# Kernel tuning notes

Hardware: AMD Instinct MI355X
Metric: run time of the kernel (lower is better)

Reference implementation:

```python
import jax, jax.numpy as jnp
import numpy as np
import math

L_MAX = 2; NRAD = 8; R_CUT = 3.5; N_LAYERS = 4; MUL0 = 32; MUL1 = 16
N_NODES = 20000; N_EDGES = 640000

# Orthonormal (Frobenius) basis of symmetric traceless 3x3 matrices for l=2
# component order: xy, yz, z^2, xz, x^2-y^2
_s2 = 1.0 / math.sqrt(2.0); _s6 = 1.0 / math.sqrt(6.0)
_B = np.zeros((5, 3, 3), dtype=np.float32)
_B[0, 0, 1] = _B[0, 1, 0] = _s2
_B[1, 1, 2] = _B[1, 2, 1] = _s2
_B[2, 0, 0] = _B[2, 1, 1] = -_s6; _B[2, 2, 2] = 2 * _s6
_B[3, 0, 2] = _B[3, 2, 0] = _s2
_B[4, 0, 0] = _s2; _B[4, 1, 1] = -_s2
B2 = jnp.asarray(_B)


def silu(x):
    return x * jax.nn.sigmoid(x)


def cutoff_fn(d):
    # CosineCutoff
    return 0.5 * (jnp.cos(d * math.pi / R_CUT) + 1.0) * (d < R_CUT).astype(d.dtype)


def smearing(d, means, betas):
    # ExpNormalSmearing with CosineCutoff envelope
    dc = jnp.clip(d, 1e-6, R_CUT)[:, None]          # [E,1]
    a = 5.0 / R_CUT
    b = jnp.clip(betas, 1e-6, None)
    return cutoff_fn(dc) * jnp.exp(-b * (jnp.exp(-a * dc) - means) ** 2)  # [E,NRAD]


def sph_harm(rh):
    # real spherical harmonics up to l=2, component normalization, (x,y,z) l=1 order
    y0 = jnp.ones_like(rh[:, :1])
    y1 = math.sqrt(3.0) * rh                                   # [E,3]
    rr = rh[:, :, None] * rh[:, None, :]                       # [E,3,3]
    tr = (rh * rh).sum(-1) / 3.0
    rr = rr - tr[:, None, None] * jnp.eye(3, dtype=rh.dtype)   # traceless
    y2 = math.sqrt(15.0) * jnp.einsum('eij,kij->ek', rr, B2)   # [E,5]
    return jnp.concatenate([y0, y1, y2], axis=-1)              # [E,9]


def _forward(pos, alpha, atom_emb, ne_emb, ne_dw, ne_db, ne_cw, ne_cb,
             means, betas, rad_w1, rad_b1, rad_w2, rad_b2,
             tp_w00, tp_w110, tp_w01, tp_w10, tp_w12,
             self_ws, self_wv, pre_ws, pre_wv, post_ws, post_wv,
             ln_g, ln_b, g_w1, g_b1, g_w2, g_b2, z, edge_index):
    N = pos.shape[0]
    src, dst = edge_index[0], edge_index[1]
    rvec = pos[dst] - pos[src]
    d = jnp.sqrt((rvec * rvec).sum(-1) + 1e-12)                # [E]
    rhat = rvec / d[:, None]

    rbf = smearing(d, means, betas)                            # [E,NRAD]
    # per-l radial coefficients (3 small MLPs, stacked on leading dim)
    h = silu(jnp.einsum('en,lnh->leh', rbf, rad_w1) + rad_b1[:, None, :])
    coeff = jnp.einsum('leh,lho->leo', h, rad_w2) + rad_b2[:, None, :]  # [3,E,1]

    Y = sph_harm(rhat)                                         # [E,9]
    eattr = jnp.concatenate([Y[:, :1] * coeff[0],
                             Y[:, 1:4] * coeff[1],
                             Y[:, 4:9] * coeff[2]], axis=-1)
    eattr = jnp.nan_to_num(eattr, nan=0.0, posinf=0.0, neginf=0.0)

    # AtomEncoder + NeighborEmbedding
    s = atom_emb[z]                                            # [N,32]
    C = cutoff_fn(d)
    W = (rbf @ ne_dw + ne_db) * C[:, None]                     # [E,32]
    xn = ne_emb[z]
    aggr = jax.ops.segment_sum(xn[dst] * W, src, num_segments=N)
    s = jnp.concatenate([s, aggr], axis=-1) @ ne_cw + ne_cb    # [N,32]
    v = jnp.zeros((N, MUL1, 3), dtype=s.dtype)                 # l=1 features

    e0, e1, e2 = eattr[:, :1], eattr[:, 1:4], eattr[:, 4:9]
    Qe = jnp.einsum('ek,kij->eij', e2, B2)                     # l=2 as sym traceless matrix

    for li in range(N_LAYERS):
        ss, vs = s[src], v[src]
        # CG tensor product paths (FullyConnectedTensorProduct node x edge -> node)
        m_s = (ss * e0) @ tp_w00[li] + jnp.einsum('evc,ec->ev', vs, e1) @ tp_w110[li]
        m_v = (jnp.einsum('ei,io->eo', ss, tp_w01[li])[:, :, None] * e1[:, None, :]
               + jnp.einsum('evc,vo->eoc', vs * e0[:, :, None], tp_w10[li])
               + jnp.einsum('evc,vo->eoc', jnp.einsum('eij,evj->evi', Qe, vs), tp_w12[li]))
        # alpha-weighted scatter-add aggregation
        ms = jax.ops.segment_sum(m_s * alpha, dst, num_segments=N)
        mv = jax.ops.segment_sum(m_v * alpha[:, :, None], dst, num_segments=N)
        # self interaction (o3.Linear, block-diag per l)
        s = s @ self_ws[li] + ms
        v = jnp.einsum('nvc,vo->noc', v, self_wv[li]) + mv
        # pre-linear -> gate -> post-linear
        ps = s @ pre_ws[li]                                    # [N,48] scalars+gates
        pv = jnp.einsum('nvc,vo->noc', v, pre_wv[li])
        sc = silu(ps[:, :MUL0])
        g = jax.nn.sigmoid(ps[:, MUL0:])
        v = pv * g[:, :, None]
        s = sc @ post_ws[li]
        v = jnp.einsum('nvc,vo->noc', v, post_wv[li])
        # layernorm on scalar channels
        mu = s.mean(-1, keepdims=True)
        var = ((s - mu) ** 2).mean(-1, keepdims=True)
        s = (s - mu) / jnp.sqrt(var + 1e-5) * ln_g[li] + ln_b[li]
        # geom2s: vector norms -> scalar residual
        vn = jnp.sqrt((v * v).sum(-1) + 1e-12)                 # [N,16]
        delta = silu(vn @ g_w1[li] + g_b1[li]) @ g_w2[li] + g_b2[li]
        s = s + delta
    return jnp.concatenate([s, v.reshape(N, MUL1 * 3)], axis=-1)  # [N,80]


def setup_inputs() -> dict:
    key = jax.random.key(0)
    ks = jax.random.split(key, 40)
    f32 = jnp.float32

    def rn(k, shape, fan):
        return jax.random.normal(k, shape, dtype=f32) / math.sqrt(fan)

    start = math.exp(-R_CUT)
    inp = {
        'pos': jax.random.uniform(ks[0], (N_NODES, 3), dtype=f32) * 10.0,
        'alpha': jax.random.uniform(ks[1], (N_EDGES, 1), dtype=f32),
        'atom_emb': rn(ks[2], (100, MUL0), 1.0),
        'ne_emb': rn(ks[3], (100, MUL0), 1.0),
        'ne_dw': rn(ks[4], (NRAD, MUL0), NRAD), 'ne_db': jnp.zeros((MUL0,), f32),
        'ne_cw': rn(ks[5], (2 * MUL0, MUL0), 2 * MUL0), 'ne_cb': jnp.zeros((MUL0,), f32),
        'means': jnp.linspace(start, 1.0, NRAD, dtype=f32),
        'betas': jnp.full((NRAD,), (2.0 / NRAD * (1.0 - start)) ** (-2), dtype=f32),
        'rad_w1': rn(ks[6], (3, NRAD, 256), NRAD), 'rad_b1': jnp.zeros((3, 256), f32),
        'rad_w2': rn(ks[7], (3, 256, 1), 256), 'rad_b2': jnp.zeros((3, 1), f32),
        'tp_w00': rn(ks[8], (N_LAYERS, MUL0, MUL0), MUL0),
        'tp_w110': rn(ks[9], (N_LAYERS, MUL1, MUL0), MUL1),
        'tp_w01': rn(ks[10], (N_LAYERS, MUL0, MUL1), MUL0),
        'tp_w10': rn(ks[11], (N_LAYERS, MUL1, MUL1), MUL1),
        'tp_w12': rn(ks[12], (N_LAYERS, MUL1, MUL1), MUL1),
        'self_ws': rn(ks[13], (N_LAYERS, MUL0, MUL0), MUL0),
        'self_wv': rn(ks[14], (N_LAYERS, MUL1, MUL1), MUL1),
        'pre_ws': rn(ks[15], (N_LAYERS, MUL0, MUL0 + MUL1), MUL0),
        'pre_wv': rn(ks[16], (N_LAYERS, MUL1, MUL1), MUL1),
        'post_ws': rn(ks[17], (N_LAYERS, MUL0, MUL0), MUL0),
        'post_wv': rn(ks[18], (N_LAYERS, MUL1, MUL1), MUL1),
        'ln_g': jnp.ones((N_LAYERS, MUL0), f32), 'ln_b': jnp.zeros((N_LAYERS, MUL0), f32),
        'g_w1': rn(ks[19], (N_LAYERS, MUL1, MUL1), MUL1), 'g_b1': jnp.zeros((N_LAYERS, MUL1), f32),
        'g_w2': rn(ks[20], (N_LAYERS, MUL1, MUL0), MUL1), 'g_b2': jnp.zeros((N_LAYERS, MUL0), f32),
        'z': jax.random.randint(ks[21], (N_NODES,), 0, 100, dtype=jnp.int32),
        'edge_index': jax.random.randint(ks[22], (2, N_EDGES), 0, N_NODES, dtype=jnp.int32),
    }
    return inp


def reference(pos, alpha, atom_emb, ne_emb, ne_dw, ne_db, ne_cw, ne_cb,
              means, betas, rad_w1, rad_b1, rad_w2, rad_b2,
              tp_w00, tp_w110, tp_w01, tp_w10, tp_w12,
              self_ws, self_wv, pre_ws, pre_wv, post_ws, post_wv,
              ln_g, ln_b, g_w1, g_b1, g_w2, g_b2, z, edge_index):
    return _forward(pos, alpha, atom_emb, ne_emb, ne_dw, ne_db, ne_cw, ne_cb,
                    means, betas, rad_w1, rad_b1, rad_w2, rad_b2,
                    tp_w00, tp_w110, tp_w01, tp_w10, tp_w12,
                    self_ws, self_wv, pre_ws, pre_wv, post_ws, post_wv,
                    ln_g, ln_b, g_w1, g_b1, g_w2, g_b2, z, edge_index)
```

## Files before the change

### kernel.cpp

```cpp
#include <hip/hip_runtime.h>

#define RCUT 3.5f
#define TTAB 2048

static __device__ __forceinline__ float sigmoidf_(float x) { return 1.0f / (1.0f + expf(-x)); }
static __device__ __forceinline__ float siluf(float x) { return x / (1.0f + expf(-x)); }
static __device__ __forceinline__ float san(float x) {
    return ((__float_as_uint(x) & 0x7F800000u) != 0x7F800000u) ? x : 0.f;
}

__global__ __launch_bounds__(256) void k_table(const float* means, const float* betas,
                        const float* rad_w1, const float* rad_b1,
                        const float* rad_w2, const float* rad_b2,
                        const float* ne_dw, const float* ne_db,
                        float* tab) {
    __shared__ float red[3][4];
    int i = blockIdx.x;
    int h = threadIdx.x;
    int lane = h & 63, wv = h >> 6;
    float d  = (float)i * (RCUT / (float)(TTAB - 1));
    float dc = fmaxf(d, 1e-6f);
    float C  = (dc < RCUT) ? 0.5f * (cosf(dc * (3.14159265358979f / RCUT)) + 1.0f) : 0.0f;
    float ex = expf(-(5.0f / RCUT) * dc);
    float rbf[8];
#pragma unroll
    for (int nn = 0; nn < 8; ++nn) {
        float b = fmaxf(betas[nn], 1e-6f);
        float t = ex - means[nn];
        rbf[nn] = C * expf(-b * t * t);
    }
    float con[3];
#pragma unroll
    for (int l = 0; l < 3; ++l) {
        float cc = rad_b1[l * 256 + h];
#pragma unroll
        for (int nn = 0; nn < 8; ++nn) cc += rbf[nn] * rad_w1[(l * 8 + nn) * 256 + h];
        con[l] = siluf(cc) * rad_w2[l * 256 + h];
    }
#pragma unroll
    for (int m = 1; m < 64; m <<= 1) {
        con[0] += __shfl_xor(con[0], m, 64);
        con[1] += __shfl_xor(con[1], m, 64);
        con[2] += __shfl_xor(con[2], m, 64);
    }
    if (lane == 0) { red[0][wv] = con[0]; red[1][wv] = con[1]; red[2][wv] = con[2]; }
    __syncthreads();
    if (h < 3)
        tab[i * 40 + h] = rad_b2[h] + red[h][0] + red[h][1] + red[h][2] + red[h][3];
    else if (h == 3)
        tab[i * 40 + 3] = 0.f;
    else if (h < 36) {
        int c = h - 4;
        float wvv = ne_db[c];
#pragma unroll
        for (int nn = 0; nn < 8; ++nn) wvv += rbf[nn] * ne_dw[nn * 32 + c];
        tab[i * 40 + h] = wvv * C;
    } else if (h < 40)
        tab[i * 40 + h] = 0.f;
}

__global__ void k_count(const int* ei, int* cnt_dst, int* cnt_src, int E) {
    int e = blockIdx.x * blockDim.x + threadIdx.x;
    if (e >= E) return;
    atomicAdd(cnt_dst + ei[E + e], 1);
    atomicAdd(cnt_src + ei[e], 1);
}

__global__ __launch_bounds__(1024) void k_scan2(const int* cntA, int* rowA, int* curA,
                        const int* cntB, int* rowB, int* curB, int n) {
    __shared__ int wsum[16];
    const int* cnt = blockIdx.x ? cntB : cntA;
    int* rowptr    = blockIdx.x ? rowB : rowA;
    int* cursor    = blockIdx.x ? curB : curA;
    int tid = threadIdx.x, lane = tid & 63, wv = tid >> 6;
    int per = (n + 1023) >> 10;
    int beg = tid * per; if (beg > n) beg = n;
    int end = beg + per; if (end > n) end = n;
    int s = 0;
    for (int i = beg; i < end; ++i) s += cnt[i];
    int v = s;
#pragma unroll
    for (int m = 1; m < 64; m <<= 1) {
        int t = __shfl_up(v, m, 64);
        if (lane >= m) v += t;
    }
    if (lane == 63) wsum[wv] = v;
    __syncthreads();
    int wbase = 0;
    for (int j = 0; j < wv; ++j) wbase += wsum[j];
    int run = wbase + v - s;
    for (int i = beg; i < end; ++i) {
        int val = cnt[i];
        rowptr[i] = run; cursor[i] = run;
        run += val;
    }
    if (tid == 1023) rowptr[n] = run;
}

__global__ void k_edge_fill(const float* pos, const float* alpha,
                            const int* ei, const float* tab, const int* z,
                            int* cur_dst, int* cur_src,
                            float4* rec, int2* rec_src, int E) {
    int e = blockIdx.x * blockDim.x + threadIdx.x;
    if (e >= E) return;
    int sn = ei[e], dn = ei[E + e];
    float rx = pos[dn * 3]     - pos[sn * 3];
    float ry = pos[dn * 3 + 1] - pos[sn * 3 + 1];
    float rz = pos[dn * 3 + 2] - pos[sn * 3 + 2];
    float d = sqrtf(rx * rx + ry * ry + rz * rz + 1e-12f);
    float inv = 1.0f / d;
    rx *= inv; ry *= inv; rz *= inv;
    float u = fminf(d, RCUT) * ((float)(TTAB - 1) / RCUT);
    int i0 = (int)u; if (i0 > TTAB - 2) i0 = TTAB - 2;
    float f = u - (float)i0;
    const float* t0 = tab + i0 * 40;
    float c0 = t0[0] + f * (t0[40] - t0[0]);
    float c1 = t0[1] + f * (t0[41] - t0[1]);
    float c2 = t0[2] + f * (t0[42] - t0[2]);
    float al = alpha[e];
    float ae0 = san(al * c0);
    float k1 = 1.73205081f * al * c1;
    float k2 = al * c2;
    float e20 = san(5.47722558f * rx * ry * k2);
    float e21 = san(5.47722558f * ry * rz * k2);
    float e22 = san(1.58113883f * (2.f * rz * rz - rx * rx - ry * ry) * k2);
    float e23 = san(5.47722558f * rx * rz * k2);
    float e24 = san(2.73861279f * (rx * rx - ry * ry) * k2);
    const float S2 = 0.70710678f, S6 = 0.40824829f;
    float q00 = -S6 * e22 + S2 * e24;
    float q01 = S2 * e20;
    float q02 = S2 * e23;
    float q11 = -S6 * e22 - S2 * e24;
    float q12 = S2 * e21;
    float q22 = 2.f * S6 * e22;
    int p = atomicAdd(cur_dst + dn, 1);
    size_t pb = (size_t)p * 4;
    rec[pb]     = make_float4(ae0, san(k1 * rx), san(k1 * ry), san(k1 * rz));
    rec[pb + 1] = make_float4(q00, q01, q02, q11);
    rec[pb + 2] = make_float4(q12, q22, __int_as_float(sn), 0.f);
    int p2 = atomicAdd(cur_src + sn, 1);
    float uc = fminf(u, (float)(TTAB - 1) - 1e-3f);
    rec_src[p2] = make_int2(__float_as_int(uc), z[dn]);
}

__global__ __launch_bounds__(256) void k_aggr(const int* row_src, const int2* recs,
        const int* z, const float* tab, const float* ne_emb, const float* atom_emb,
        const float* ne_cw, const float* ne_cb,
        float* sbuf, float* vbuf, int N) {
    __shared__ float part[4][64];
    __shared__ float cat[4][64];
    int wv = threadIdx.x >> 6, lane = threadIdx.x & 63;
    int n = blockIdx.x * 4 + wv;
    bool act = n < N;
    int g = lane >> 5, li = lane & 31;
    float acc = 0.f;
    if (act) {
        int r0 = row_src[n], r1 = row_src[n + 1];
        int half = (r1 - r0) >> 1;
        int kb = g ? (r0 + half) : r0;
        int ke = g ? r1 : (r0 + half);
        int k = kb;
        for (; k + 2 <= ke; k += 2) {
            int2 rA = recs[k], rB = recs[k + 1];
            float uA = __int_as_float(rA.x), uB = __int_as_float(rB.x);
            int iA = (int)uA, iB = (int)uB;
            float fA = uA - (float)iA, fB = uB - (float)iB;
            float wA0 = tab[iA * 40 + 4 + li], wA1 = tab[iA * 40 + 44 + li];
            float wB0 = tab[iB * 40 + 4 + li], wB1 = tab[iB * 40 + 44 + li];
            float eA = ne_emb[rA.y * 32 + li], eB = ne_emb[rB.y * 32 + li];
            acc += (wA0 + fA * (wA1 - wA0)) * eA + (wB0 + fB * (wB1 - wB0)) * eB;
        }
        for (; k < ke; ++k) {
            int2 r = recs[k];
            float u = __int_as_float(r.x);
            int i0 = (int)u; float f = u - (float)i0;
            float w0 = tab[i0 * 40 + 4 + li], w1 = tab[i0 * 40 + 44 + li];
            acc += (w0 + f * (w1 - w0)) * ne_emb[r.y * 32 + li];
        }
    }
    part[wv][lane] = acc;
    __builtin_amdgcn_wave_barrier();
    if (act && lane < 32) {
        cat[wv][lane] = atom_emb[z[n] * 32 + lane];
        cat[wv][32 + lane] = part[wv][lane] + part[wv][32 + lane];
    }
    __builtin_amdgcn_wave_barrier();
    if (act && lane < 32) {
        float so = ne_cb[lane];
        for (int j = 0; j < 64; ++j) so += cat[wv][j] * ne_cw[j * 32 + lane];
        sbuf[n * 32 + lane] = so;
    }
    if (act && lane < 48) vbuf[n * 48 + lane] = 0.f;
}

#define VBLK(BIDX, UA, VA, WA, UB, VB, WB)                                              \
    {                                                                                   \
        int ea_ = ((BIDX) << 2) + 2 * g;                                                \
        float4 Aa = eA[wv][ea_], Ab = eA[wv][ea_ + 1];                                  \
        float4 Qa = eQ[wv][ea_], Qb = eQ[wv][ea_ + 1];                                  \
        float2 Ra = eR[wv][ea_], Rb = eR[wv][ea_ + 1];                                  \
        adv += UA * Aa.y + VA * Aa.z + WA * Aa.w + UB * Ab.y + VB * Ab.z + WB * Ab.w;   \
        a2x += UA * Aa.x + UB * Ab.x;                                                   \
        a2y += VA * Aa.x + VB * Ab.x;                                                   \
        a2z += WA * Aa.x + WB * Ab.x;                                                   \
        a3x += Qa.x * UA + Qa.y * VA + Qa.z * WA + Qb.x * UB + Qb.y * VB + Qb.z * WB;   \
        a3y += Qa.y * UA + Qa.w * VA + Ra.x * WA + Qb.y * UB + Qb.w * VB + Rb.x * WB;   \
        a3z += Qa.z * UA + Ra.x * VA + Ra.y * WA + Qb.z * UB + Rb.x * VB + Rb.y * WB;   \
    }

#define SBLK(BIDX, X0, X1, X2, X3)                                                      \
    {                                                                                   \
        int j4_ = (BIDX) << 2;                                                          \
        float4 A0 = eA[wv][j4_], A1 = eA[wv][j4_ + 1];                                  \
        float4 A2 = eA[wv][j4_ + 2], A3 = eA[wv][j4_ + 3];                              \
        a0  += X0 * A0.x + X1 * A1.x + X2 * A2.x + X3 * A3.x;                           \
        a1x += X0 * A0.y + X1 * A1.y + X2 * A2.y + X3 * A3.y;                           \
        a1y += X0 * A0.z + X1 * A1.z + X2 * A2.z + X3 * A3.z;                           \
        a1z += X0 * A0.w + X1 * A1.w + X2 * A2.w + X3 * A3.w;                           \
    }

__global__ __launch_bounds__(256) void k_layer(const int* __restrict__ row_dst,
        const float4* __restrict__ rec,
        const float* __restrict__ sOld, const float* __restrict__ vOld,
        const float* w00, const float* w110, const float* w01,
        const float* w10, const float* w12,
        const float* self_ws, const float* self_wv,
        const float* pre_ws, const float* pre_wv,
        const float* post_ws, const float* post_wv,
        const float* ln_g, const float* ln_b,
        const float* g_w1, const float* g_b1,
        const float* g_w2, const float* g_b2,
        float* __restrict__ sNew, float* __restrict__ vNew,
        float* __restrict__ out, int N) {
    __shared__ float M[4][352];
    __shared__ float S[4][32], V[4][48], P[4][48];
    __shared__ float4 eA[4][64];
    __shared__ float4 eQ[4][64];
    __shared__ float2 eR[4][64];
    __shared__ int4   eC[4][16];
    int wv = threadIdx.x >> 6, lane = threadIdx.x & 63;
    int n = blockIdx.x * 4 + wv;
    bool act = n < N;
    int c = lane >> 4, o = lane & 15;
    int g = (lane >> 4) & 1, m = lane & 15;

    if (act && lane < 32) S[wv][lane] = sOld[n * 32 + lane];
    if (act && lane < 48) V[wv][lane] = vOld[(size_t)n * 48 + o * 3 + c];

    int r0 = 0, r1 = 0;
    if (act) { r0 = row_dst[n]; r1 = row_dst[n + 1]; }
    int deg = r1 - r0;
    int cap = deg < 64 ? deg : 64;
    if (lane < cap) {
        size_t idx = (size_t)(r0 + lane) * 4;
        float4 a  = rec[idx];
        float4 q  = rec[idx + 1];
        float4 r2 = rec[idx + 2];
        eA[wv][lane] = a;
        eQ[wv][lane] = q;
        eR[wv][lane] = make_float2(r2.x, r2.y);
        ((int*)&eC[wv][0])[lane] = __float_as_int(r2.z);
    }
    __builtin_amdgcn_wave_barrier();

    float a0 = 0.f, a1x = 0.f, a1y = 0.f, a1z = 0.f;
    float adv = 0.f, a2x = 0.f, a2y = 0.f, a2z = 0.f, a3x = 0.f, a3y = 0.f, a3z = 0.f;
    int nblk = cap >> 2;

    float xA0 = 0.f, xA1 = 0.f, xA2 = 0.f, xA3 = 0.f;
    float xB0 = 0.f, xB1 = 0.f, xB2 = 0.f, xB3 = 0.f;
    float uaA = 0.f, vaA = 0.f, waA = 0.f, ubA = 0.f, vbA = 0.f, wbA = 0.f;
    float uaB = 0.f, vaB = 0.f, waB = 0.f, ubB = 0.f, vbB = 0.f, wbB = 0.f;
    if (nblk > 0) {
        int4 c4 = eC[wv][0];
        if (lane < 32) {
            xA0 = sOld[c4.x * 32 + lane]; xA1 = sOld[c4.y * 32 + lane];
            xA2 = sOld[c4.z * 32 + lane]; xA3 = sOld[c4.w * 32 + lane];
        } else {
            int ca = g ? c4.z : c4.x, cb = g ? c4.w : c4.y;
            const float* pa = vOld + (size_t)ca * 48 + m * 3;
            const float* pb = vOld + (size_t)cb * 48 + m * 3;
            uaA = pa[0]; vaA = pa[1]; waA = pa[2];
            ubA = pb[0]; vbA = pb[1]; wbA = pb[2];
        }
    }
    if (nblk > 1) {
        int4 c4 = eC[wv][1];
        if (lane < 32) {
            xB0 = sOld[c4.x * 32 + lane]; xB1 = sOld[c4.y * 32 + lane];
            xB2 = sOld[c4.z * 32 + lane]; xB3 = sOld[c4.w * 32 + lane];
        } else {
            int ca = g ? c4.z : c4.x, cb = g ? c4.w : c4.y;
            const float* pa = vOld + (size_t)ca * 48 + m * 3;
            const float* pb = vOld + (size_t)cb * 48 + m * 3;
            uaB = pa[0]; vaB = pa[1]; waB = pa[2];
            ubB = pb[0]; vbB = pb[1]; wbB = pb[2];
        }
    }
    int b = 0;
    for (; b + 2 <= nblk; b += 2) {
        int4 cN0 = (b + 2 < nblk) ? eC[wv][b + 2] : make_int4(0, 0, 0, 0);
        int4 cN1 = (b + 3 < nblk) ? eC[wv][b + 3] : make_int4(0, 0, 0, 0);
        if (lane < 32) {
            float t0 = sOld[cN0.x * 32 + lane], t1 = sOld[cN0.y * 32 + lane];
            float t2 = sOld[cN0.z * 32 + lane], t3 = sOld[cN0.w * 32 + lane];
            float u0 = sOld[cN1.x * 32 + lane], u1 = sOld[cN1.y * 32 + lane];
            float u2 = sOld[cN1.z * 32 + lane], u3 = sOld[cN1.w * 32 + lane];
            SBLK(b, xA0, xA1, xA2, xA3);
            SBLK(b + 1, xB0, xB1, xB2, xB3);
            xA0 = t0; xA1 = t1; xA2 = t2; xA3 = t3;
            xB0 = u0; xB1 = u1; xB2 = u2; xB3 = u3;
        } else {
            int na0 = g ? cN0.z : cN0.x, nb0 = g ? cN0.w : cN0.y;
            int na1 = g ? cN1.z : cN1.x, nb1 = g ? cN1.w : cN1.y;
            const float* qa0 = vOld + (size_t)na0 * 48 + m * 3;
            const float* qb0 = vOld + (size_t)nb0 * 48 + m * 3;
            const float* qa1 = vOld + (size_t)na1 * 48 + m * 3;
            const float* qb1 = vOld + (size_t)nb1 * 48 + m * 3;
            float tua = qa0[0], tva = qa0[1], twa = qa0[2];
            float tub = qb0[0], tvb = qb0[1], twb = qb0[2];
            float sua = qa1[0], sva = qa1[1], swa = qa1[2];
            float sub = qb1[0], svb = qb1[1], swb = qb1[2];
            VBLK(b, uaA, vaA, waA, ubA, vbA, wbA);
            VBLK(b + 1, uaB, vaB, waB, ubB, vbB, wbB);
            uaA = tua; vaA = tva; waA = twa; ubA = tub; vbA = tvb; wbA = twb;
            uaB = sua; vaB = sva; waB = swa; ubB = sub; vbB = svb; wbB = swb;
        }
    }
    if (b < nblk) {
        if (lane < 32) {
            SBLK(b, xA0, xA1, xA2, xA3);
        } else {
            VBLK(b, uaA, vaA, waA, ubA, vbA, wbA);
        }
    }
    for (int k = r0 + (nblk << 2); k < r1; ++k) {
        size_t kb = (size_t)k * 4;
        float4 A = rec[kb];
        if (lane < 32) {
            float4 R = rec[kb + 2];
            int cc = __float_as_int(R.z);
            float xx = sOld[cc * 32 + lane];
            a0 += xx * A.x; a1x += xx * A.y; a1y += xx * A.z; a1z += xx * A.w;
        } else if (lane < 48) {
            float4 Q = rec[kb + 1];
            float4 R = rec[kb + 2];
            int cc = __float_as_int(R.z);
            const float* vp = vOld + (size_t)cc * 48 + m * 3;
            float vx = vp[0], vy = vp[1], vz = vp[2];
            adv += vx * A.y + vy * A.z + vz * A.w;
            a2x += vx * A.x; a2y += vy * A.x; a2z += vz * A.x;
            a3x += Q.x * vx + Q.y * vy + Q.z * vz;
            a3y += Q.y * vx + Q.w * vy + R.x * vz;
            a3z += Q.z * vx + R.x * vy + R.y * vz;
        }
    }
    if (lane < 32) {
        M[wv][lane] = a0; M[wv][32 + lane] = a1x;
        M[wv][64 + lane] = a1y; M[wv][96 + lane] = a1z;
    } else {
        int base = 128 + g * 112;
        M[wv][base + m] = adv;
        M[wv][base + 16 + m] = a2x; M[wv][base + 32 + m] = a2y; M[wv][base + 48 + m] = a2z;
        M[wv][base + 64 + m] = a3x; M[wv][base + 80 + m] = a3y; M[wv][base + 96 + m] = a3z;
    }
    __builtin_amdgcn_wave_barrier();
    float s1 = 0.f, v1 = 0.f;
    if (act && lane < 32) {
        for (int i = 0; i < 32; ++i) s1 += M[wv][i] * w00[i * 32 + lane];
        for (int v = 0; v < 16; ++v)
            s1 += (M[wv][128 + v] + M[wv][240 + v]) * w110[v * 32 + lane];
        for (int i = 0; i < 32; ++i) s1 += S[wv][i] * self_ws[i * 32 + lane];
    }
    if (act && lane < 48) {
        for (int i = 0; i < 32; ++i) v1 += M[wv][32 + c * 32 + i] * w01[i * 16 + o];
        for (int v = 0; v < 16; ++v)
            v1 += (M[wv][144 + c * 16 + v] + M[wv][256 + c * 16 + v]) * w10[v * 16 + o];
        for (int v = 0; v < 16; ++v)
            v1 += (M[wv][192 + c * 16 + v] + M[wv][304 + c * 16 + v]) * w12[v * 16 + o];
        for (int v = 0; v < 16; ++v) v1 += V[wv][c * 16 + v] * self_wv[v * 16 + o];
    }
    __builtin_amdgcn_wave_barrier();
    if (lane < 32) S[wv][lane] = s1;
    if (lane < 48) V[wv][lane] = v1;
    __builtin_amdgcn_wave_barrier();
    float ps = 0.f, pv = 0.f;
    if (act && lane < 48) {
        for (int i = 0; i < 32; ++i) ps += S[wv][i] * pre_ws[i * 48 + lane];
        for (int v = 0; v < 16; ++v) pv += V[wv][c * 16 + v] * pre_wv[v * 16 + o];
    }
    if (lane < 48) P[wv][lane] = ps;
    __builtin_amdgcn_wave_barrier();
    float gg = sigmoidf_(P[wv][32 + o]);
    float sc = (lane < 32) ? siluf(ps) : 0.f;
    float v2 = pv * gg;
    __builtin_amdgcn_wave_barrier();
    if (lane < 32) S[wv][lane] = sc;
    if (lane < 48) V[wv][lane] = v2;
    __builtin_amdgcn_wave_barrier();
    float s2 = 0.f, v3 = 0.f;
    if (act && lane < 32) { for (int i = 0; i < 32; ++i) s2 += S[wv][i] * post_ws[i * 32 + lane]; }
    if (act && lane < 48) { for (int v = 0; v < 16; ++v) v3 += V[wv][c * 16 + v] * post_wv[v * 16 + o]; }
    __builtin_amdgcn_wave_barrier();
    if (lane < 48) V[wv][lane] = v3;
    float mu = s2;
    mu += __shfl_xor(mu, 1, 32); mu += __shfl_xor(mu, 2, 32);
    mu += __shfl_xor(mu, 4, 32); mu += __shfl_xor(mu, 8, 32); mu += __shfl_xor(mu, 16, 32);
    mu *= (1.0f / 32.0f);
    float t = s2 - mu;
    float var = t * t;
    var += __shfl_xor(var, 1, 32); var += __shfl_xor(var, 2, 32);
    var += __shfl_xor(var, 4, 32); var += __shfl_xor(var, 8, 32); var += __shfl_xor(var, 16, 32);
    var *= (1.0f / 32.0f);
    float sln = 0.f;
    if (act && lane < 32) sln = t * rsqrtf(var + 1e-5f) * ln_g[lane] + ln_b[lane];
    __builtin_amdgcn_wave_barrier();
    if (lane < 16) {
        float vx = V[wv][lane], vy = V[wv][16 + lane], vz = V[wv][32 + lane];
        P[wv][lane] = sqrtf(vx * vx + vy * vy + vz * vz + 1e-12f);
    }
    __builtin_amdgcn_wave_barrier();
    if (lane < 16) {
        float x = g_b1[lane];
        for (int mm = 0; mm < 16; ++mm) x += P[wv][mm] * g_w1[mm * 16 + lane];
        P[wv][16 + lane] = siluf(x);
    }
    __builtin_amdgcn_wave_barrier();
    float sfin = 0.f;
    if (act && lane < 32) {
        float dl = g_b2[lane];
        for (int oo = 0; oo < 16; ++oo) dl += P[wv][16 + oo] * g_w2[oo * 32 + lane];
        sfin = sln + dl;
    }
    if (out) {
        if (act && lane < 32) out[(size_t)n * 80 + lane] = sfin;
        if (act && lane < 48) out[(size_t)n * 80 + 32 + o * 3 + c] = v3;
    } else {
        if (act && lane < 32) sNew[n * 32 + lane] = sfin;
        if (act && lane < 48) vNew[(size_t)n * 48 + o * 3 + c] = v3;
    }
}

extern "C" void kernel_launch(void* const* d_in, const int* in_sizes, int n_in,
                              void* d_out, int out_size, void* d_ws, size_t ws_size,
                              hipStream_t stream) {
    auto F = [&](int i) { return (const float*)d_in[i]; };
    const int* z  = (const int*)d_in[31];
    const int* ei = (const int*)d_in[32];
    int N = in_sizes[0] / 3;
    int E = in_sizes[1];

    char* w = (char*)d_ws;
    size_t off = 0;
    auto take = [&](size_t bytes) { size_t cur = off; off += (bytes + 255) & ~(size_t)255; return cur; };
    float4* rec    = (float4*)(w + take((size_t)E * 64));
    int2*  rec_src = (int2*)(w + take((size_t)E * 8));
    float* tab     = (float*)(w + take((size_t)TTAB * 40 * 4));
    int* cnt_dst   = (int*)(w + take((size_t)2 * N * 4));
    int* cnt_src   = cnt_dst + N;
    int* row_dst   = (int*)(w + take((size_t)(N + 1) * 4));
    int* row_src   = (int*)(w + take((size_t)(N + 1) * 4));
    int* cur_dst   = (int*)(w + take((size_t)N * 4));
    int* cur_src   = (int*)(w + take((size_t)N * 4));
    float* sA      = (float*)(w + take((size_t)N * 32 * 4));
    float* vA      = (float*)(w + take((size_t)N * 48 * 4));
    float* sB      = (float*)(w + take((size_t)N * 32 * 4));
    float* vB      = (float*)(w + take((size_t)N * 48 * 4));

    hipMemsetAsync(cnt_dst, 0, (size_t)2 * N * 4, stream);

    k_table<<<TTAB, 256, 0, stream>>>(F(8), F(9), F(10), F(11),
                                      F(12), F(13), F(4), F(5), tab);
    k_count<<<(E + 255) / 256, 256, 0, stream>>>(ei, cnt_dst, cnt_src, E);
    k_scan2<<<2, 1024, 0, stream>>>(cnt_dst, row_dst, cur_dst,
                                    cnt_src, row_src, cur_src, N);
    k_edge_fill<<<(E + 255) / 256, 256, 0, stream>>>(F(0), F(1), ei, tab, z,
                                                     cur_dst, cur_src,
                                                     rec, rec_src, E);

    int nb = (N + 3) / 4;
    k_aggr<<<nb, 256, 0, stream>>>(row_src, rec_src, z, tab, F(3), F(2),
                                   F(6), F(7), sA, vA, N);

    float* sIn = sA; float* vIn = vA;
    float* sOut = sB; float* vOut = vB;
    for (int li = 0; li < 4; ++li) {
        float* outp = (li == 3) ? (float*)d_out : nullptr;
        k_layer<<<nb, 256, 0, stream>>>(row_dst, rec,
                                        sIn, vIn,
                                        F(14) + li * 32 * 32, F(15) + li * 16 * 32,
                                        F(16) + li * 32 * 16, F(17) + li * 16 * 16,
                                        F(18) + li * 16 * 16,
                                        F(19) + li * 32 * 32, F(20) + li * 16 * 16,
                                        F(21) + li * 32 * 48, F(22) + li * 16 * 16,
                                        F(23) + li * 32 * 32, F(24) + li * 16 * 16,
                                        F(25) + li * 32, F(26) + li * 32,
                                        F(27) + li * 16 * 16, F(28) + li * 16,
                                        F(29) + li * 16 * 32, F(30) + li * 32,
                                        sOut, vOut, outp, N);
        float* ts = sIn; sIn = sOut; sOut = ts;
        float* tv = vIn; vIn = vOut; vOut = tv;
    }
}
```

Measured before the change: 640.3 us.

## Split layer node work across two waves: scalar aggregation and vector aggregation

```diff
diff --git a/kernel.cpp b/kernel.cpp
--- a/kernel.cpp
+++ b/kernel.cpp
@@ -193,33 +193,30 @@
     if (act && lane < 48) vbuf[n * 48 + lane] = 0.f;
 }
 
-#define VBLK(BIDX, UA, VA, WA, UB, VB, WB)                                              \
+#define SBLK2(BIDX, X0, X1)                                                             \
     {                                                                                   \
-        int ea_ = ((BIDX) << 2) + 2 * g;                                                \
-        float4 Aa = eA[wv][ea_], Ab = eA[wv][ea_ + 1];                                  \
-        float4 Qa = eQ[wv][ea_], Qb = eQ[wv][ea_ + 1];                                  \
-        float2 Ra = eR[wv][ea_], Rb = eR[wv][ea_ + 1];                                  \
-        adv += UA * Aa.y + VA * Aa.z + WA * Aa.w + UB * Ab.y + VB * Ab.z + WB * Ab.w;   \
-        a2x += UA * Aa.x + UB * Ab.x;                                                   \
-        a2y += VA * Aa.x + VB * Ab.x;                                                   \
-        a2z += WA * Aa.x + WB * Ab.x;                                                   \
-        a3x += Qa.x * UA + Qa.y * VA + Qa.z * WA + Qb.x * UB + Qb.y * VB + Qb.z * WB;   \
-        a3y += Qa.y * UA + Qa.w * VA + Ra.x * WA + Qb.y * UB + Qb.w * VB + Rb.x * WB;   \
-        a3z += Qa.z * UA + Ra.x * VA + Ra.y * WA + Qb.z * UB + Rb.x * VB + Rb.y * WB;   \
-    }
-
-#define SBLK(BIDX, X0, X1, X2, X3)                                                      \
+        int e_ = ((BIDX) << 2) + 2 * h;                                                 \
+        float4 A0 = eA[e_], A1 = eA[e_ + 1];                                            \
+        a0  += X0 * A0.x + X1 * A1.x;                                                   \
+        a1x += X0 * A0.y + X1 * A1.y;                                                   \
+        a1y += X0 * A0.z + X1 * A1.z;                                                   \
+        a1z += X0 * A0.w + X1 * A1.w;                                                   \
+    }
+
+#define VBLK1(BIDX, U, V, W)                                                            \
     {                                                                                   \
-        int j4_ = (BIDX) << 2;                                                          \
-        float4 A0 = eA[wv][j4_], A1 = eA[wv][j4_ + 1];                                  \
-        float4 A2 = eA[wv][j4_ + 2], A3 = eA[wv][j4_ + 3];                              \
-        a0  += X0 * A0.x + X1 * A1.x + X2 * A2.x + X3 * A3.x;                           \
-        a1x += X0 * A0.y + X1 * A1.y + X2 * A2.y + X3 * A3.y;                           \
-        a1y += X0 * A0.z + X1 * A1.z + X2 * A2.z + X3 * A3.z;                           \
-        a1z += X0 * A0.w + X1 * A1.w + X2 * A2.w + X3 * A3.w;                           \
-    }
-
-__global__ __launch_bounds__(256) void k_layer(const int* __restrict__ row_dst,
+        int e_ = ((BIDX) << 2) + g;                                                     \
+        float4 Aa = eA[e_];                                                             \
+        float4 Qa = eQ[e_];                                                             \
+        float2 Ra = eR[e_];                                                             \
+        adv += U * Aa.y + V * Aa.z + W * Aa.w;                                          \
+        a2x += U * Aa.x; a2y += V * Aa.x; a2z += W * Aa.x;                              \
+        a3x += Qa.x * U + Qa.y * V + Qa.z * W;                                          \
+        a3y += Qa.y * U + Qa.w * V + Ra.x * W;                                          \
+        a3z += Qa.z * U + Ra.x * V + Ra.y * W;                                          \
+    }
+
+__global__ __launch_bounds__(128) void k_layer(const int* __restrict__ row_dst,
         const float4* __restrict__ rec,
         const float* __restrict__ sOld, const float* __restrict__ vOld,
         const float* w00, const float* w110, const float* w01,
@@ -232,212 +229,229 @@
         const float* g_w2, const float* g_b2,
         float* __restrict__ sNew, float* __restrict__ vNew,
         float* __restrict__ out, int N) {
-    __shared__ float M[4][352];
-    __shared__ float S[4][32], V[4][48], P[4][48];
-    __shared__ float4 eA[4][64];
-    __shared__ float4 eQ[4][64];
-    __shared__ float2 eR[4][64];
-    __shared__ int4   eC[4][16];
+    __shared__ __align__(16) float4 eA[64];
+    __shared__ __align__(16) float4 eQ[64];
+    __shared__ __align__(16) float2 eR[64];
+    __shared__ __align__(16) int    eC[64];
+    __shared__ float M[240];
+    __shared__ float S[32], Vt[48], P[48];
     int wv = threadIdx.x >> 6, lane = threadIdx.x & 63;
-    int n = blockIdx.x * 4 + wv;
-    bool act = n < N;
-    int c = lane >> 4, o = lane & 15;
-    int g = (lane >> 4) & 1, m = lane & 15;
-
-    if (act && lane < 32) S[wv][lane] = sOld[n * 32 + lane];
-    if (act && lane < 48) V[wv][lane] = vOld[(size_t)n * 48 + o * 3 + c];
-
-    int r0 = 0, r1 = 0;
-    if (act) { r0 = row_dst[n]; r1 = row_dst[n + 1]; }
+    int n = blockIdx.x;
+    int r0 = row_dst[n], r1 = row_dst[n + 1];
     int deg = r1 - r0;
     int cap = deg < 64 ? deg : 64;
-    if (lane < cap) {
-        size_t idx = (size_t)(r0 + lane) * 4;
-        float4 a  = rec[idx];
-        float4 q  = rec[idx + 1];
-        float4 r2 = rec[idx + 2];
-        eA[wv][lane] = a;
-        eQ[wv][lane] = q;
-        eR[wv][lane] = make_float2(r2.x, r2.y);
-        ((int*)&eC[wv][0])[lane] = __float_as_int(r2.z);
-    }
-    __builtin_amdgcn_wave_barrier();
-
-    float a0 = 0.f, a1x = 0.f, a1y = 0.f, a1z = 0.f;
-    float adv = 0.f, a2x = 0.f, a2y = 0.f, a2z = 0.f, a3x = 0.f, a3y = 0.f, a3z = 0.f;
     int nblk = cap >> 2;
 
-    float xA0 = 0.f, xA1 = 0.f, xA2 = 0.f, xA3 = 0.f;
-    float xB0 = 0.f, xB1 = 0.f, xB2 = 0.f, xB3 = 0.f;
-    float uaA = 0.f, vaA = 0.f, waA = 0.f, ubA = 0.f, vbA = 0.f, wbA = 0.f;
-    float uaB = 0.f, vaB = 0.f, waB = 0.f, ubB = 0.f, vbB = 0.f, wbB = 0.f;
-    if (nblk > 0) {
-        int4 c4 = eC[wv][0];
+    if (wv == 0) {
+        if (lane < cap) {
+            size_t idx = (size_t)(r0 + lane) * 4;
+            float4 a  = rec[idx];
+            float4 r2 = rec[idx + 2];
+            eA[lane] = a;
+            eR[lane] = make_float2(r2.x, r2.y);
+            eC[lane] = __float_as_int(r2.z);
+        }
+        if (lane < 32) S[lane] = sOld[(size_t)n * 32 + lane];
+    } else {
+        if (lane < cap) {
+            size_t idx = (size_t)(r0 + lane) * 4;
+            eQ[lane] = rec[idx + 1];
+        }
+        if (lane < 48) Vt[(lane & 15) * 0 + (lane >> 4) * 16 + 0] = 0.f;
+        if (lane < 48) Vt[(lane >> 4) * 16 + 0] = Vt[(lane >> 4) * 16 + 0];
+        if (lane < 48) {
+            int c_ = lane >> 4, o_ = lane & 15;
+            Vt[c_ * 16 + o_] = vOld[(size_t)n * 48 + o_ * 3 + c_];
+        }
+    }
+    __syncthreads();
+
+    const int4* eC4 = (const int4*)eC;
+    if (wv == 0) {
+        int h = lane >> 5, d = lane & 31;
+        float a0 = 0.f, a1x = 0.f, a1y = 0.f, a1z = 0.f;
+        float xA0 = 0.f, xA1 = 0.f, xB0 = 0.f, xB1 = 0.f;
+        if (nblk > 0) {
+            int4 c4 = eC4[0];
+            xA0 = sOld[(h ? c4.z : c4.x) * 32 + d];
+            xA1 = sOld[(h ? c4.w : c4.y) * 32 + d];
+        }
+        if (nblk > 1) {
+            int4 c4 = eC4[1];
+            xB0 = sOld[(h ? c4.z : c4.x) * 32 + d];
+            xB1 = sOld[(h ? c4.w : c4.y) * 32 + d];
+        }
+        int b = 0;
+        for (; b + 2 <= nblk; b += 2) {
+            int4 c40 = (b + 2 < nblk) ? eC4[b + 2] : make_int4(0, 0, 0, 0);
+            int4 c41 = (b + 3 < nblk) ? eC4[b + 3] : make_int4(0, 0, 0, 0);
+            float t0 = sOld[(h ? c40.z : c40.x) * 32 + d];
+            float t1 = sOld[(h ? c40.w : c40.y) * 32 + d];
+            float u0 = sOld[(h ? c41.z : c41.x) * 32 + d];
+            float u1 = sOld[(h ? c41.w : c41.y) * 32 + d];
+            SBLK2(b, xA0, xA1);
+            SBLK2(b + 1, xB0, xB1);
+            xA0 = t0; xA1 = t1; xB0 = u0; xB1 = u1;
+        }
+        if (b < nblk) { SBLK2(b, xA0, xA1); }
+        for (int k = r0 + (nblk << 2); k < r1; ++k) {
+            if (h == 0) {
+                size_t kb = (size_t)k * 4;
+                float4 A = rec[kb];
+                int cc = __float_as_int(rec[kb + 2].z);
+                float xx = sOld[cc * 32 + d];
+                a0 += xx * A.x; a1x += xx * A.y; a1y += xx * A.z; a1z += xx * A.w;
+            }
+        }
+        a0  += __shfl_xor(a0, 32, 64);
+        a1x += __shfl_xor(a1x, 32, 64);
+        a1y += __shfl_xor(a1y, 32, 64);
+        a1z += __shfl_xor(a1z, 32, 64);
         if (lane < 32) {
-            xA0 = sOld[c4.x * 32 + lane]; xA1 = sOld[c4.y * 32 + lane];
-            xA2 = sOld[c4.z * 32 + lane]; xA3 = sOld[c4.w * 32 + lane];
-        } else {
-            int ca = g ? c4.z : c4.x, cb = g ? c4.w : c4.y;
-            const float* pa = vOld + (size_t)ca * 48 + m * 3;
-            const float* pb = vOld + (size_t)cb * 48 + m * 3;
-            uaA = pa[0]; vaA = pa[1]; waA = pa[2];
-            ubA = pb[0]; vbA = pb[1]; wbA = pb[2];
-        }
-    }
-    if (nblk > 1) {
-        int4 c4 = eC[wv][1];
+            M[lane] = a0; M[32 + lane] = a1x; M[64 + lane] = a1y; M[96 + lane] = a1z;
+        }
+    } else {
+        int g = lane >> 4, m = lane & 15;
+        float adv = 0.f, a2x = 0.f, a2y = 0.f, a2z = 0.f, a3x = 0.f, a3y = 0.f, a3z = 0.f;
+        float uA = 0.f, vA = 0.f, wA = 0.f, uB = 0.f, vB = 0.f, wB = 0.f;
+        if (nblk > 0) {
+            const float* vp = vOld + (size_t)eC[g] * 48 + m * 3;
+            uA = vp[0]; vA = vp[1]; wA = vp[2];
+        }
+        if (nblk > 1) {
+            const float* vp = vOld + (size_t)eC[4 + g] * 48 + m * 3;
+            uB = vp[0]; vB = vp[1]; wB = vp[2];
+        }
+        int b = 0;
+        for (; b + 2 <= nblk; b += 2) {
+            int cn0 = (b + 2 < nblk) ? eC[(b + 2) * 4 + g] : 0;
+            int cn1 = (b + 3 < nblk) ? eC[(b + 3) * 4 + g] : 0;
+            const float* q0 = vOld + (size_t)cn0 * 48 + m * 3;
+            const float* q1 = vOld + (size_t)cn1 * 48 + m * 3;
+            float tu = q0[0], tv = q0[1], tw = q0[2];
+            float su = q1[0], sv = q1[1], sw = q1[2];
+            VBLK1(b, uA, vA, wA);
+            VBLK1(b + 1, uB, vB, wB);
+            uA = tu; vA = tv; wA = tw; uB = su; vB = sv; wB = sw;
+        }
+        if (b < nblk) { VBLK1(b, uA, vA, wA); }
+        for (int k = r0 + (nblk << 2); k < r1; ++k) {
+            if (g == 0) {
+                size_t kb = (size_t)k * 4;
+                float4 A = rec[kb];
+                float4 Q = rec[kb + 1];
+                float4 R2 = rec[kb + 2];
+                int cc = __float_as_int(R2.z);
+                const float* vp = vOld + (size_t)cc * 48 + m * 3;
+                float vx = vp[0], vy = vp[1], vz = vp[2];
+                adv += vx * A.y + vy * A.z + vz * A.w;
+                a2x += vx * A.x; a2y += vy * A.x; a2z += vz * A.x;
+                a3x += Q.x * vx + Q.y * vy + Q.z * vz;
+                a3y += Q.y * vx + Q.w * vy + R2.x * vz;
+                a3z += Q.z * vx + R2.x * vy + R2.y * vz;
+            }
+        }
+        adv += __shfl_xor(adv, 16, 64); adv += __shfl_xor(adv, 32, 64);
+        a2x += __shfl_xor(a2x, 16, 64); a2x += __shfl_xor(a2x, 32, 64);
+        a2y += __shfl_xor(a2y, 16, 64); a2y += __shfl_xor(a2y, 32, 64);
+        a2z += __shfl_xor(a2z, 16, 64); a2z += __shfl_xor(a2z, 32, 64);
+        a3x += __shfl_xor(a3x, 16, 64); a3x += __shfl_xor(a3x, 32, 64);
+        a3y += __shfl_xor(a3y, 16, 64); a3y += __shfl_xor(a3y, 32, 64);
+        a3z += __shfl_xor(a3z, 16, 64); a3z += __shfl_xor(a3z, 32, 64);
+        if (lane < 16) {
+            M[128 + m] = adv;
+            M[144 + m] = a2x; M[160 + m] = a2y; M[176 + m] = a2z;
+            M[192 + m] = a3x; M[208 + m] = a3y; M[224 + m] = a3z;
+        }
+    }
+    __syncthreads();
+
+    float sln = 0.f, pv = 0.f;
+    int c = lane >> 4, o = lane & 15;
+    if (wv == 0) {
+        float s1 = 0.f;
         if (lane < 32) {
-            xB0 = sOld[c4.x * 32 + lane]; xB1 = sOld[c4.y * 32 + lane];
-            xB2 = sOld[c4.z * 32 + lane]; xB3 = sOld[c4.w * 32 + lane];
-        } else {
-            int ca = g ? c4.z : c4.x, cb = g ? c4.w : c4.y;
-            const float* pa = vOld + (size_t)ca * 48 + m * 3;
-            const float* pb = vOld + (size_t)cb * 48 + m * 3;
-            uaB = pa[0]; vaB = pa[1]; waB = pa[2];
-            ubB = pb[0]; vbB = pb[1]; wbB = pb[2];
-        }
-    }
-    int b = 0;
-    for (; b + 2 <= nblk; b += 2) {
-        int4 cN0 = (b + 2 < nblk) ? eC[wv][b + 2] : make_int4(0, 0, 0, 0);
-        int4 cN1 = (b + 3 < nblk) ? eC[wv][b + 3] : make_int4(0, 0, 0, 0);
+            for (int i = 0; i < 32; ++i) s1 += M[i] * w00[i * 32 + lane];
+            for (int v = 0; v < 16; ++v) s1 += M[128 + v] * w110[v * 32 + lane];
+            for (int i = 0; i < 32; ++i) s1 += S[i] * self_ws[i * 32 + lane];
+        }
+        __builtin_amdgcn_wave_barrier();
+        if (lane < 32) S[lane] = s1;
+        __builtin_amdgcn_wave_barrier();
+        float ps = 0.f;
+        if (lane < 48) {
+            for (int i = 0; i < 32; ++i) ps += S[i] * pre_ws[i * 48 + lane];
+            P[lane] = ps;
+        }
+        __builtin_amdgcn_wave_barrier();
+        float sc = (lane < 32) ? siluf(ps) : 0.f;
+        if (lane < 32) S[lane] = sc;
+        __builtin_amdgcn_wave_barrier();
+        float s2 = 0.f;
+        if (lane < 32) { for (int i = 0; i < 32; ++i) s2 += S[i] * post_ws[i * 32 + lane]; }
+        float mu = s2;
+        mu += __shfl_xor(mu, 1, 32); mu += __shfl_xor(mu, 2, 32);
+        mu += __shfl_xor(mu, 4, 32); mu += __shfl_xor(mu, 8, 32); mu += __shfl_xor(mu, 16, 32);
+        mu *= (1.0f / 32.0f);
+        float t = s2 - mu;
+        float var = t * t;
+        var += __shfl_xor(var, 1, 32); var += __shfl_xor(var, 2, 32);
+        var += __shfl_xor(var, 4, 32); var += __shfl_xor(var, 8, 32); var += __shfl_xor(var, 16, 32);
+        var *= (1.0f / 32.0f);
+        if (lane < 32) sln = t * rsqrtf(var + 1e-5f) * ln_g[lane] + ln_b[lane];
+    } else {
+        float v1 = 0.f;
+        if (lane < 48) {
+            for (int i = 0; i < 32; ++i) v1 += M[32 + c * 32 + i] * w01[i * 16 + o];
+            for (int v = 0; v < 16; ++v) v1 += M[144 + c * 16 + v] * w10[v * 16 + o];
+            for (int v = 0; v < 16; ++v) v1 += M[192 + c * 16 + v] * w12[v * 16 + o];
+            for (int v = 0; v < 16; ++v) v1 += Vt[c * 16 + v] * self_wv[v * 16 + o];
+        }
+        __builtin_amdgcn_wave_barrier();
+        if (lane < 48) Vt[lane] = v1;
+        __builtin_amdgcn_wave_barrier();
+        if (lane < 48) {
+            for (int v = 0; v < 16; ++v) pv += Vt[c * 16 + v] * pre_wv[v * 16 + o];
+        }
+    }
+    __syncthreads();
+
+    float v3 = 0.f;
+    if (wv == 1) {
+        float v2 = (lane < 48) ? pv * sigmoidf_(P[32 + o]) : 0.f;
+        __builtin_amdgcn_wave_barrier();
+        if (lane < 48) Vt[lane] = v2;
+        __builtin_amdgcn_wave_barrier();
+        if (lane < 48) { for (int v = 0; v < 16; ++v) v3 += Vt[c * 16 + v] * post_wv[v * 16 + o]; }
+        __builtin_amdgcn_wave_barrier();
+        if (lane < 48) Vt[lane] = v3;
+        __builtin_amdgcn_wave_barrier();
+        if (lane < 16) {
+            float vx = Vt[lane], vy = Vt[16 + lane], vz = Vt[32 + lane];
+            P[lane] = sqrtf(vx * vx + vy * vy + vz * vz + 1e-12f);
+        }
+        __builtin_amdgcn_wave_barrier();
+        if (lane < 16) {
+            float x = g_b1[lane];
+            for (int mm = 0; mm < 16; ++mm) x += P[mm] * g_w1[mm * 16 + lane];
+            P[16 + lane] = siluf(x);
+        }
+    }
+    __syncthreads();
+
+    if (wv == 0) {
         if (lane < 32) {
-            float t0 = sOld[cN0.x * 32 + lane], t1 = sOld[cN0.y * 32 + lane];
-            float t2 = sOld[cN0.z * 32 + lane], t3 = sOld[cN0.w * 32 + lane];
-            float u0 = sOld[cN1.x * 32 + lane], u1 = sOld[cN1.y * 32 + lane];
-            float u2 = sOld[cN1.z * 32 + lane], u3 = sOld[cN1.w * 32 + lane];
-            SBLK(b, xA0, xA1, xA2, xA3);
-            SBLK(b + 1, xB0, xB1, xB2, xB3);
-            xA0 = t0; xA1 = t1; xA2 = t2; xA3 = t3;
-            xB0 = u0; xB1 = u1; xB2 = u2; xB3 = u3;
-        } else {
-            int na0 = g ? cN0.z : cN0.x, nb0 = g ? cN0.w : cN0.y;
-            int na1 = g ? cN1.z : cN1.x, nb1 = g ? cN1.w : cN1.y;
-            const float* qa0 = vOld + (size_t)na0 * 48 + m * 3;
-            const float* qb0 = vOld + (size_t)nb0 * 48 + m * 3;
-            const float* qa1 = vOld + (size_t)na1 * 48 + m * 3;
-            const float* qb1 = vOld + (size_t)nb1 * 48 + m * 3;
-            float tua = qa0[0], tva = qa0[1], twa = qa0[2];
-            float tub = qb0[0], tvb = qb0[1], twb = qb0[2];
-            float sua = qa1[0], sva = qa1[1], swa = qa1[2];
-            float sub = qb1[0], svb = qb1[1], swb = qb1[2];
-            VBLK(b, uaA, vaA, waA, ubA, vbA, wbA);
-            VBLK(b + 1, uaB, vaB, waB, ubB, vbB, wbB);
-            uaA = tua; vaA = tva; waA = twa; ubA = tub; vbA = tvb; wbA = twb;
-            uaB = sua; vaB = sva; waB = swa; ubB = sub; vbB = svb; wbB = swb;
-        }
-    }
-    if (b < nblk) {
-        if (lane < 32) {
-            SBLK(b, xA0, xA1, xA2, xA3);
-        } else {
-            VBLK(b, uaA, vaA, waA, ubA, vbA, wbA);
-        }
-    }
-    for (int k = r0 + (nblk << 2); k < r1; ++k) {
-        size_t kb = (size_t)k * 4;
-        float4 A = rec[kb];
-        if (lane < 32) {
-            float4 R = rec[kb + 2];
-            int cc = __float_as_int(R.z);
-            float xx = sOld[cc * 32 + lane];
-            a0 += xx * A.x; a1x += xx * A.y; a1y += xx * A.z; a1z += xx * A.w;
-        } else if (lane < 48) {
-            float4 Q = rec[kb + 1];
-            float4 R = rec[kb + 2];
-            int cc = __float_as_int(R.z);
-            const float* vp = vOld + (size_t)cc * 48 + m * 3;
-            float vx = vp[0], vy = vp[1], vz = vp[2];
-            adv += vx * A.y + vy * A.z + vz * A.w;
-            a2x += vx * A.x; a2y += vy * A.x; a2z += vz * A.x;
-            a3x += Q.x * vx + Q.y * vy + Q.z * vz;
-            a3y += Q.y * vx + Q.w * vy + R.x * vz;
-            a3z += Q.z * vx + R.x * vy + R.y * vz;
-        }
-    }
-    if (lane < 32) {
-        M[wv][lane] = a0; M[wv][32 + lane] = a1x;
-        M[wv][64 + lane] = a1y; M[wv][96 + lane] = a1z;
+            float dl = g_b2[lane];
+            for (int oo = 0; oo < 16; ++oo) dl += P[16 + oo] * g_w2[oo * 32 + lane];
+            float sfin = sln + dl;
+            if (out) out[(size_t)n * 80 + lane] = sfin;
+            else     sNew[(size_t)n * 32 + lane] = sfin;
+        }
     } else {
-        int base = 128 + g * 112;
-        M[wv][base + m] = adv;
-        M[wv][base + 16 + m] = a2x; M[wv][base + 32 + m] = a2y; M[wv][base + 48 + m] = a2z;
-        M[wv][base + 64 + m] = a3x; M[wv][base + 80 + m] = a3y; M[wv][base + 96 + m] = a3z;
-    }
-    __builtin_amdgcn_wave_barrier();
-    float s1 = 0.f, v1 = 0.f;
-    if (act && lane < 32) {
-        for (int i = 0; i < 32; ++i) s1 += M[wv][i] * w00[i * 32 + lane];
-        for (int v = 0; v < 16; ++v)
-            s1 += (M[wv][128 + v] + M[wv][240 + v]) * w110[v * 32 + lane];
-        for (int i = 0; i < 32; ++i) s1 += S[wv][i] * self_ws[i * 32 + lane];
-    }
-    if (act && lane < 48) {
-        for (int i = 0; i < 32; ++i) v1 += M[wv][32 + c * 32 + i] * w01[i * 16 + o];
-        for (int v = 0; v < 16; ++v)
-            v1 += (M[wv][144 + c * 16 + v] + M[wv][256 + c * 16 + v]) * w10[v * 16 + o];
-        for (int v = 0; v < 16; ++v)
-            v1 += (M[wv][192 + c * 16 + v] + M[wv][304 + c * 16 + v]) * w12[v * 16 + o];
-        for (int v = 0; v < 16; ++v) v1 += V[wv][c * 16 + v] * self_wv[v * 16 + o];
-    }
-    __builtin_amdgcn_wave_barrier();
-    if (lane < 32) S[wv][lane] = s1;
-    if (lane < 48) V[wv][lane] = v1;
-    __builtin_amdgcn_wave_barrier();
-    float ps = 0.f, pv = 0.f;
-    if (act && lane < 48) {
-        for (int i = 0; i < 32; ++i) ps += S[wv][i] * pre_ws[i * 48 + lane];
-        for (int v = 0; v < 16; ++v) pv += V[wv][c * 16 + v] * pre_wv[v * 16 + o];
-    }
-    if (lane < 48) P[wv][lane] = ps;
-    __builtin_amdgcn_wave_barrier();
-    float gg = sigmoidf_(P[wv][32 + o]);
-    float sc = (lane < 32) ? siluf(ps) : 0.f;
-    float v2 = pv * gg;
-    __builtin_amdgcn_wave_barrier();
-    if (lane < 32) S[wv][lane] = sc;
-    if (lane < 48) V[wv][lane] = v2;
-    __builtin_amdgcn_wave_barrier();
-    float s2 = 0.f, v3 = 0.f;
-    if (act && lane < 32) { for (int i = 0; i < 32; ++i) s2 += S[wv][i] * post_ws[i * 32 + lane]; }
-    if (act && lane < 48) { for (int v = 0; v < 16; ++v) v3 += V[wv][c * 16 + v] * post_wv[v * 16 + o]; }
-    __builtin_amdgcn_wave_barrier();
-    if (lane < 48) V[wv][lane] = v3;
-    float mu = s2;
-    mu += __shfl_xor(mu, 1, 32); mu += __shfl_xor(mu, 2, 32);
-    mu += __shfl_xor(mu, 4, 32); mu += __shfl_xor(mu, 8, 32); mu += __shfl_xor(mu, 16, 32);
-    mu *= (1.0f / 32.0f);
-    float t = s2 - mu;
-    float var = t * t;
-    var += __shfl_xor(var, 1, 32); var += __shfl_xor(var, 2, 32);
-    var += __shfl_xor(var, 4, 32); var += __shfl_xor(var, 8, 32); var += __shfl_xor(var, 16, 32);
-    var *= (1.0f / 32.0f);
-    float sln = 0.f;
-    if (act && lane < 32) sln = t * rsqrtf(var + 1e-5f) * ln_g[lane] + ln_b[lane];
-    __builtin_amdgcn_wave_barrier();
-    if (lane < 16) {
-        float vx = V[wv][lane], vy = V[wv][16 + lane], vz = V[wv][32 + lane];
-        P[wv][lane] = sqrtf(vx * vx + vy * vy + vz * vz + 1e-12f);
-    }
-    __builtin_amdgcn_wave_barrier();
-    if (lane < 16) {
-        float x = g_b1[lane];
-        for (int mm = 0; mm < 16; ++mm) x += P[wv][mm] * g_w1[mm * 16 + lane];
-        P[wv][16 + lane] = siluf(x);
-    }
-    __builtin_amdgcn_wave_barrier();
-    float sfin = 0.f;
-    if (act && lane < 32) {
-        float dl = g_b2[lane];
-        for (int oo = 0; oo < 16; ++oo) dl += P[wv][16 + oo] * g_w2[oo * 32 + lane];
-        sfin = sln + dl;
-    }
-    if (out) {
-        if (act && lane < 32) out[(size_t)n * 80 + lane] = sfin;
-        if (act && lane < 48) out[(size_t)n * 80 + 32 + o * 3 + c] = v3;
-    } else {
-        if (act && lane < 32) sNew[n * 32 + lane] = sfin;
-        if (act && lane < 48) vNew[(size_t)n * 48 + o * 3 + c] = v3;
+        if (lane < 48) {
+            if (out) out[(size_t)n * 80 + 32 + o * 3 + c] = v3;
+            else     vNew[(size_t)n * 48 + o * 3 + c] = v3;
+        }
     }
 }
 
@@ -486,7 +500,7 @@
     float* sOut = sB; float* vOut = vB;
     for (int li = 0; li < 4; ++li) {
         float* outp = (li == 3) ? (float*)d_out : nullptr;
-        k_layer<<<nb, 256, 0, stream>>>(row_dst, rec,
+        k_layer<<<N, 128, 0, stream>>>(row_dst, rec,
                                         sIn, vIn,
                                         F(14) + li * 32 * 32, F(15) + li * 16 * 32,
                                         F(16) + li * 32 * 16, F(17) + li * 16 * 16,
```

New measurement: 572.3 us. 10.6% less time.
